# Optimization experiments

Hardware: AMD Instinct MI355X
Metric: run time of the kernel (lower is better)

Reference implementation:

```python
import jax, jax.numpy as jnp
import numpy as np

VOCAB, D_MODEL, N_STATE, H_HEADS, LAYERS = 64, 512, 32, 16, 4
EXPAND = 2
D_INNER = EXPAND * D_MODEL          # 1024
P_HEAD = D_INNER // H_HEADS         # 64
CONV_DIM = D_INNER + 2 * N_STATE    # x, B, C share the depthwise conv
K_CONV = 4
D_IN_PROJ = 2 * D_INNER + 2 * N_STATE + H_HEADS  # z, x, B, C, dt
BATCH, SEQ = 4, 1024
EPS = 1e-5


def rmsnorm(x, w):
    return x * jax.lax.rsqrt(jnp.mean(x * x, axis=-1, keepdims=True) + EPS) * w


def silu(x):
    return x * jax.nn.sigmoid(x)


def causal_depthwise_conv(x, w, b):
    # x: [B,L,C], w: [C,K], b: [C]; causal (left) padding, depthwise groups
    xt = jnp.transpose(x, (0, 2, 1))  # [B,C,L]
    out = jax.lax.conv_general_dilated(xt, w[:, None, :], (1,), [(K_CONV - 1, 0)], feature_group_count=w.shape[0])
    return jnp.transpose(out, (0, 2, 1)) + b


def ssd(xh, dt, A, Bm, Cm, Dp):
    # Mamba2 SSD recurrence. xh [B,L,H,P], dt [B,L,H], A [H], Bm/Cm [B,L,N], Dp [H]
    dA = jnp.exp(dt * A)              # decay per (batch, step, head)
    dtx = dt[..., None] * xh          # [B,L,H,P]

    def step(h, inp):
        dA_t, dtx_t, B_t, C_t = inp
        # h: [B,H,P,N]
        h = dA_t[:, :, None, None] * h + dtx_t[..., None] * B_t[:, None, None, :]
        y = jnp.einsum('bhpn,bn->bhp', h, C_t)
        return h, y

    h0 = jnp.zeros((xh.shape[0], H_HEADS, P_HEAD, N_STATE), xh.dtype)
    _, ys = jax.lax.scan(step, h0, (jnp.moveaxis(dA, 1, 0), jnp.moveaxis(dtx, 1, 0), jnp.moveaxis(Bm, 1, 0), jnp.moveaxis(Cm, 1, 0)))
    return jnp.moveaxis(ys, 0, 1) + xh * Dp[None, None, :, None]


def mamba_block(x, norm_w, W_in, b_in, conv_w, conv_b, dt_bias, A_log, Dp, gnorm_w, W_out, b_out):
    res = x
    u = rmsnorm(x, norm_w)
    zxbcdt = u @ W_in + b_in                                # [B,L,D_IN_PROJ]
    z = zxbcdt[..., :D_INNER]
    xBC = zxbcdt[..., D_INNER:D_INNER + CONV_DIM]
    dt = zxbcdt[..., D_INNER + CONV_DIM:]                   # [B,L,H]
    xBC = silu(causal_depthwise_conv(xBC, conv_w, conv_b))
    xc = xBC[..., :D_INNER]
    Bm = xBC[..., D_INNER:D_INNER + N_STATE]
    Cm = xBC[..., D_INNER + N_STATE:]
    dt = jax.nn.softplus(dt + dt_bias)
    xh = xc.reshape(xc.shape[0], xc.shape[1], H_HEADS, P_HEAD)
    y = ssd(xh, dt, -jnp.exp(A_log), Bm, Cm, Dp)
    y = y.reshape(y.shape[0], y.shape[1], D_INNER)
    y = rmsnorm(y * silu(z), gnorm_w)                       # gated RMSNorm
    return res + y @ W_out + b_out


def forward(input_tokens, emb, norm_w, W_in, b_in, conv_w, conv_b, dt_bias, A_log, D_param, gnorm_w, W_out, b_out, head_w, head_b):
    h = emb[input_tokens]
    for i in range(LAYERS):
        h = mamba_block(h, norm_w[i], W_in[i], b_in[i], conv_w[i], conv_b[i], dt_bias[i], A_log[i], D_param[i], gnorm_w[i], W_out[i], b_out[i])
    return h @ head_w + head_b


def setup_inputs() -> dict:
    key = jax.random.key(0)
    ks = jax.random.split(key, 8)
    s = 0.02
    return {
        'input_tokens': jax.random.randint(ks[0], (BATCH, SEQ), 0, VOCAB),
        'emb': jax.random.normal(ks[1], (VOCAB, D_MODEL), jnp.float32) * s,
        'norm_w': jnp.ones((LAYERS, D_MODEL), jnp.float32),
        'W_in': jax.random.normal(ks[2], (LAYERS, D_MODEL, D_IN_PROJ), jnp.float32) * s,
        'b_in': jnp.zeros((LAYERS, D_IN_PROJ), jnp.float32),
        'conv_w': jax.random.normal(ks[3], (LAYERS, CONV_DIM, K_CONV), jnp.float32) * 0.1,
        'conv_b': jnp.zeros((LAYERS, CONV_DIM), jnp.float32),
        'dt_bias': jnp.tile(jnp.log(jnp.expm1(jnp.linspace(0.001, 0.1, H_HEADS, dtype=jnp.float32))), (LAYERS, 1)),
        'A_log': jnp.tile(jnp.log(jnp.arange(1, H_HEADS + 1, dtype=jnp.float32)), (LAYERS, 1)),
        'D_param': jnp.ones((LAYERS, H_HEADS), jnp.float32),
        'gnorm_w': jnp.ones((LAYERS, D_INNER), jnp.float32),
        'W_out': jax.random.normal(ks[4], (LAYERS, D_INNER, D_MODEL), jnp.float32) * s,
        'b_out': jnp.zeros((LAYERS, D_MODEL), jnp.float32),
        'head_w': jax.random.normal(ks[5], (D_MODEL, VOCAB), jnp.float32) * s,
        'head_b': jnp.zeros((VOCAB,), jnp.float32),
    }


def reference(input_tokens, emb, norm_w, W_in, b_in, conv_w, conv_b, dt_bias, A_log, D_param, gnorm_w, W_out, b_out, head_w, head_b):
    return forward(input_tokens, emb, norm_w, W_in, b_in, conv_w, conv_b, dt_bias, A_log, D_param, gnorm_w, W_out, b_out, head_w, head_b)
```

## Files before the change

kernel.cpp:

```cpp
#include <hip/hip_runtime.h>
#include <hip/hip_bf16.h>

#define VOCAB     64
#define D_MODEL   512
#define N_STATE   32
#define H_HEADS   16
#define LAYERS    4
#define D_INNER   1024
#define P_HEAD    64
#define CONV_DIM  1088
#define K_CONV    4
#define D_IN_PROJ 2128
#define NPAD_IN   2176
#define NPAD_HEAD 128
#define BATCH     4
#define SEQ       1024
#define NTOK      (BATCH*SEQ)
#define EPS       1e-5f
#define CL        64
#define NC        (SEQ/CL)
#define PSTR      80

typedef __bf16 bf16x8 __attribute__((ext_vector_type(8)));
typedef float  f32x4  __attribute__((ext_vector_type(4)));

__device__ __forceinline__ float sigmoidf_(float x) { return 1.f / (1.f + __expf(-x)); }
__device__ __forceinline__ float softplusf_(float x) { return (x > 20.f) ? x : log1pf(__expf(x)); }

__global__ void rmsnorm512_kernel(const float* __restrict__ x, const float* __restrict__ w,
                                  __bf16* __restrict__ out,
                                  const int* __restrict__ tok, const float* __restrict__ emb,
                                  float* __restrict__ hout) {
  int tokid = blockIdx.x;
  int tid = threadIdx.x;
  float v0, v1;
  if (tok) {
    const float* er = emb + (size_t)tok[tokid] * D_MODEL;
    v0 = er[tid]; v1 = er[tid + 256];
    float* hr = hout + (size_t)tokid * D_MODEL;
    hr[tid] = v0; hr[tid + 256] = v1;
  } else {
    const float* xr = x + (size_t)tokid * D_MODEL;
    v0 = xr[tid]; v1 = xr[tid + 256];
  }
  float ss = v0 * v0 + v1 * v1;
  #pragma unroll
  for (int o = 32; o >= 1; o >>= 1) ss += __shfl_xor(ss, o);
  __shared__ float red[4];
  if ((tid & 63) == 0) red[tid >> 6] = ss;
  __syncthreads();
  float tot = red[0] + red[1] + red[2] + red[3];
  float sc = rsqrtf(tot * (1.f / D_MODEL) + EPS);
  out[(size_t)tokid * D_MODEL + tid]       = (__bf16)(v0 * sc * w[tid]);
  out[(size_t)tokid * D_MODEL + tid + 256] = (__bf16)(v1 * sc * w[tid + 256]);
}

__global__ void transpose_cast_kernel(const float* __restrict__ W, __bf16* __restrict__ Wt,
                                      int K, int N, int Npad) {
  W  += (size_t)blockIdx.z * K * N;
  Wt += (size_t)blockIdx.z * Npad * K;
  __shared__ float T[32][33];
  int n0 = blockIdx.x * 32, k0 = blockIdx.y * 32;
  int tx = threadIdx.x & 31, ty = threadIdx.x >> 5;
  #pragma unroll
  for (int i = 0; i < 4; i++) {
    int n = n0 + tx;
    T[ty + i * 8][tx] = (n < N) ? W[(size_t)(k0 + ty + i * 8) * N + n] : 0.f;
  }
  __syncthreads();
  #pragma unroll
  for (int i = 0; i < 4; i++)
    Wt[(size_t)(n0 + ty + i * 8) * K + k0 + tx] = (__bf16)T[tx][ty + i * 8];
}

#define TM 64
#define TN 128
#define TK 64
__global__ __launch_bounds__(256) void gemm_bf16_kernel(
    const __bf16* __restrict__ A, const __bf16* __restrict__ Bt,
    const float* __restrict__ bias, const float* __restrict__ res,
    float* __restrict__ C, __bf16* __restrict__ Cbf, int K, int N, int ldc) {
  __shared__ __bf16 As[TM * TK];
  __shared__ __bf16 Bs[TN * TK];
  int tid = threadIdx.x;
  int lane = tid & 63, wave = tid >> 6;
  int wm = wave >> 1, wn = wave & 1;
  int q = lane >> 4, l16 = lane & 15;
  size_t row0 = (size_t)blockIdx.y * TM;
  int col0 = blockIdx.x * TN;
  const __bf16* Ab = A + row0 * K;
  const __bf16* Bb = Bt + (size_t)col0 * K;

  bf16x8 pa[2], pb[4];
  #pragma unroll
  for (int r = 0; r < 2; r++) {
    int lin = r * 256 + tid;
    pa[r] = *(const bf16x8*)(Ab + (size_t)(lin >> 3) * K + (lin & 7) * 8);
  }
  #pragma unroll
  for (int r = 0; r < 4; r++) {
    int lin = r * 256 + tid;
    pb[r] = *(const bf16x8*)(Bb + (size_t)(lin >> 3) * K + (lin & 7) * 8);
  }

  f32x4 acc[2][4];
  #pragma unroll
  for (int i = 0; i < 2; i++)
    #pragma unroll
    for (int j = 0; j < 4; j++) acc[i][j] = (f32x4){0.f, 0.f, 0.f, 0.f};

  for (int k0 = 0; k0 < K; k0 += TK) {
    #pragma unroll
    for (int r = 0; r < 2; r++) { int lin = r * 256 + tid; *(bf16x8*)(As + lin * 8) = pa[r]; }
    #pragma unroll
    for (int r = 0; r < 4; r++) { int lin = r * 256 + tid; *(bf16x8*)(Bs + lin * 8) = pb[r]; }
    __syncthreads();
    int kn = k0 + TK;
    if (kn < K) {
      #pragma unroll
      for (int r = 0; r < 2; r++) {
        int lin = r * 256 + tid;
        pa[r] = *(const bf16x8*)(Ab + (size_t)(lin >> 3) * K + kn + (lin & 7) * 8);
      }
      #pragma unroll
      for (int r = 0; r < 4; r++) {
        int lin = r * 256 + tid;
        pb[r] = *(const bf16x8*)(Bb + (size_t)(lin >> 3) * K + kn + (lin & 7) * 8);
      }
    }
    #pragma unroll
    for (int ks = 0; ks < 2; ks++) {
      bf16x8 af[2], bfv[4];
      #pragma unroll
      for (int i = 0; i < 2; i++)
        af[i] = *(const bf16x8*)(As + (wm * 32 + i * 16 + l16) * TK + ks * 32 + q * 8);
      #pragma unroll
      for (int j = 0; j < 4; j++)
        bfv[j] = *(const bf16x8*)(Bs + (wn * 64 + j * 16 + l16) * TK + ks * 32 + q * 8);
      #pragma unroll
      for (int i = 0; i < 2; i++)
        #pragma unroll
        for (int j = 0; j < 4; j++)
          acc[i][j] = __builtin_amdgcn_mfma_f32_16x16x32_bf16(af[i], bfv[j], acc[i][j], 0, 0, 0);
    }
    __syncthreads();
  }

  #pragma unroll
  for (int i = 0; i < 2; i++) {
    size_t mrow = row0 + wm * 32 + i * 16 + q * 4;
    #pragma unroll
    for (int j = 0; j < 4; j++) {
      int col = col0 + wn * 64 + j * 16 + l16;
      if (col < N) {
        float bv = bias ? bias[col] : 0.f;
        #pragma unroll
        for (int rr = 0; rr < 4; rr++) {
          size_t off = (mrow + rr) * (size_t)ldc + col;
          float v = acc[i][j][rr] + bv;
          if (res) v += res[off];
          if (C)   C[off] = v;
          if (Cbf) Cbf[off] = (__bf16)v;
        }
      }
    }
  }
}

__global__ __launch_bounds__(256) void gemm_bf16_128(
    const __bf16* __restrict__ A, const __bf16* __restrict__ Bt,
    const float* __restrict__ bias, __bf16* __restrict__ Cbf,
    int K, int N, int ldc) {
  __shared__ __bf16 As[128 * TK];
  __shared__ __bf16 Bs[128 * TK];
  int tid = threadIdx.x;
  int lane = tid & 63, wave = tid >> 6;
  int wm = wave >> 1, wn = wave & 1;
  int q = lane >> 4, l16 = lane & 15;
  size_t row0 = (size_t)blockIdx.y * 128;
  int col0 = blockIdx.x * 128;
  const __bf16* Ab = A + row0 * K;
  const __bf16* Bb = Bt + (size_t)col0 * K;

  bf16x8 pa[4], pb[4];
  #pragma unroll
  for (int r = 0; r < 4; r++) {
    int lin = r * 256 + tid;
    pa[r] = *(const bf16x8*)(Ab + (size_t)(lin >> 3) * K + (lin & 7) * 8);
    pb[r] = *(const bf16x8*)(Bb + (size_t)(lin >> 3) * K + (lin & 7) * 8);
  }

  f32x4 acc[4][4];
  #pragma unroll
  for (int i = 0; i < 4; i++)
    #pragma unroll
    for (int j = 0; j < 4; j++) acc[i][j] = (f32x4){0.f, 0.f, 0.f, 0.f};

  for (int k0 = 0; k0 < K; k0 += TK) {
    #pragma unroll
    for (int r = 0; r < 4; r++) {
      int lin = r * 256 + tid;
      *(bf16x8*)(As + lin * 8) = pa[r];
      *(bf16x8*)(Bs + lin * 8) = pb[r];
    }
    __syncthreads();
    int kn = k0 + TK;
    if (kn < K) {
      #pragma unroll
      for (int r = 0; r < 4; r++) {
        int lin = r * 256 + tid;
        pa[r] = *(const bf16x8*)(Ab + (size_t)(lin >> 3) * K + kn + (lin & 7) * 8);
        pb[r] = *(const bf16x8*)(Bb + (size_t)(lin >> 3) * K + kn + (lin & 7) * 8);
      }
    }
    #pragma unroll
    for (int ks = 0; ks < 2; ks++) {
      bf16x8 af[4], bfv[4];
      #pragma unroll
      for (int i = 0; i < 4; i++)
        af[i] = *(const bf16x8*)(As + (wm * 64 + i * 16 + l16) * TK + ks * 32 + q * 8);
      #pragma unroll
      for (int j = 0; j < 4; j++)
        bfv[j] = *(const bf16x8*)(Bs + (wn * 64 + j * 16 + l16) * TK + ks * 32 + q * 8);
      #pragma unroll
      for (int i = 0; i < 4; i++)
        #pragma unroll
        for (int j = 0; j < 4; j++)
          acc[i][j] = __builtin_amdgcn_mfma_f32_16x16x32_bf16(af[i], bfv[j], acc[i][j], 0, 0, 0);
    }
    __syncthreads();
  }

  #pragma unroll
  for (int i = 0; i < 4; i++) {
    size_t mrow = row0 + wm * 64 + i * 16 + q * 4;
    #pragma unroll
    for (int j = 0; j < 4; j++) {
      int col = col0 + wn * 64 + j * 16 + l16;
      if (col < N) {
        float bv = bias[col];
        #pragma unroll
        for (int rr = 0; rr < 4; rr++)
          Cbf[(mrow + rr) * (size_t)ldc + col] = (__bf16)(acc[i][j][rr] + bv);
      }
    }
  }
}

__device__ __forceinline__ void wave0_dt_cumsum(
    const __bf16* __restrict__ zxbf, const float* __restrict__ dt_bias,
    int b, int h, int t0, int tid, float* ldt, float* lcs) {
  if (tid < 64) {
    float dv = (float)zxbf[((size_t)(b * SEQ + t0 + tid)) * D_IN_PROJ + 2 * D_INNER + 2 * N_STATE + h]
               + dt_bias[h];
    float dtv = softplusf_(dv);
    float cs = dtv;
    #pragma unroll
    for (int off = 1; off < 64; off <<= 1) {
      float o = __shfl_up(cs, off);
      if (tid >= off) cs += o;
    }
    ldt[tid] = dtv;
    lcs[tid] = cs;
  }
}

__global__ __launch_bounds__(256) void ssd_local_kernel(
    const __bf16* __restrict__ zxbf, const float* __restrict__ conv_w,
    const float* __restrict__ conv_b, const float* __restrict__ dt_bias,
    const float* __restrict__ A_log,
    float* __restrict__ Slocal, float* __restrict__ dAprod) {
  int blk = blockIdx.x;
  int c = blk % NC;
  int h = (blk / NC) % H_HEADS;
  int b = blk / (NC * H_HEADS);
  int tid = threadIdx.x;
  int lane = tid & 63, wave = tid >> 6;
  int q = lane >> 4, l16 = lane & 15;
  int t0 = c * CL;
  float A = -__expf(A_log[h]);
  __shared__ __bf16 rawx[68][64];
  __shared__ __bf16 rawB[68][32];
  __shared__ __bf16 lxT[64][PSTR];
  __shared__ __bf16 lBT[32][PSTR];
  __shared__ float ldt[64], lcs[64];
  for (int i = tid; i < 68 * 8; i += 256) {
    int r = i >> 3, c0 = (i & 7) * 8;
    int gr = t0 - 3 + r;
    bf16x8 v;
    #pragma unroll
    for (int k = 0; k < 8; k++) v[k] = (__bf16)0.f;
    if (gr >= 0)
      v = *(const bf16x8*)(zxbf + ((size_t)(b * SEQ + gr)) * D_IN_PROJ + D_INNER + h * 64 + c0);
    *(bf16x8*)(&rawx[r][c0]) = v;
  }
  for (int i = tid; i < 68 * 4; i += 256) {
    int r = i >> 2, c0 = (i & 3) * 8;
    int gr = t0 - 3 + r;
    bf16x8 v;
    #pragma unroll
    for (int k = 0; k < 8; k++) v[k] = (__bf16)0.f;
    if (gr >= 0)
      v = *(const bf16x8*)(zxbf + ((size_t)(b * SEQ + gr)) * D_IN_PROJ + 2 * D_INNER + c0);
    *(bf16x8*)(&rawB[r][c0]) = v;
  }
  wave0_dt_cumsum(zxbf, dt_bias, b, h, t0, tid, ldt, lcs);
  __syncthreads();
  float cs63 = lcs[63];
  {
    int p = tid & 63;
    const float* w = conv_w + (h * 64 + p) * K_CONV;
    float w0 = w[0], w1 = w[1], w2 = w[2], w3 = w[3];
    float cb = conv_b[h * 64 + p];
    for (int i = tid; i < CL * 64; i += 256) {
      int t = i >> 6;
      float a = cb + w0 * (float)rawx[t][p] + w1 * (float)rawx[t + 1][p]
                   + w2 * (float)rawx[t + 2][p] + w3 * (float)rawx[t + 3][p];
      lxT[p][t] = (__bf16)(a * sigmoidf_(a));
    }
  }
  {
    int n = tid & 31;
    const float* w = conv_w + (D_INNER + n) * K_CONV;
    float w0 = w[0], w1 = w[1], w2 = w[2], w3 = w[3];
    float cb = conv_b[D_INNER + n];
    for (int i = tid; i < CL * 32; i += 256) {
      int t = i >> 5;
      float a = cb + w0 * (float)rawB[t][n] + w1 * (float)rawB[t + 1][n]
                   + w2 * (float)rawB[t + 2][n] + w3 * (float)rawB[t + 3][n];
      float v = a * sigmoidf_(a);
      float wt = ldt[t] * __expf(A * (cs63 - lcs[t]));
      lBT[n][t] = (__bf16)(v * wt);
    }
  }
  __syncthreads();
  f32x4 acc[2];
  acc[0] = (f32x4){0.f,0.f,0.f,0.f}; acc[1] = (f32x4){0.f,0.f,0.f,0.f};
  #pragma unroll
  for (int kb = 0; kb < 2; kb++) {
    bf16x8 af = *(const bf16x8*)(&lxT[wave * 16 + l16][kb * 32 + q * 8]);
    #pragma unroll
    for (int j = 0; j < 2; j++) {
      bf16x8 bf = *(const bf16x8*)(&lBT[l16 + 16 * j][kb * 32 + q * 8]);
      acc[j] = __builtin_amdgcn_mfma_f32_16x16x32_bf16(af, bf, acc[j], 0, 0, 0);
    }
  }
  float* dst = Slocal + (size_t)blk * 2048;
  #pragma unroll
  for (int j = 0; j < 2; j++) {
    int n = l16 + 16 * j;
    #pragma unroll
    for (int rr = 0; rr < 4; rr++) {
      int p = wave * 16 + q * 4 + rr;
      dst[p * 32 + n] = acc[j][rr];
    }
  }
  if (tid == 0) dAprod[blk] = __expf(A * cs63);
}

__global__ __launch_bounds__(256) void ssd_out_kernel(
    const __bf16* __restrict__ zxbf, const float* __restrict__ conv_w,
    const float* __restrict__ conv_b, const float* __restrict__ dt_bias,
    const float* __restrict__ A_log, const float* __restrict__ Dp,
    const float* __restrict__ Slocal, const float* __restrict__ dAprod,
    __bf16* __restrict__ y) {
  int blk = blockIdx.x;
  int c = blk % NC;
  int h = (blk / NC) % H_HEADS;
  int b = blk / (NC * H_HEADS);
  int tid = threadIdx.x;
  int lane = tid & 63, wave = tid >> 6;
  int q = lane >> 4, l16 = lane & 15;
  int t0 = c * CL;
  float A = -__expf(A_log[h]);
  float D = Dp[h];
  __shared__ __bf16 rawbuf[2 * 68 * 64];
  __shared__ __bf16 lxT[64][PSTR];
  __shared__ __bf16 lB[64][32];
  __shared__ __bf16 lC[64][32];
  __shared__ __bf16 lS[64][32];
  __shared__ float ldt[64], lcs[64];
  __shared__ float pr[NC];
  __bf16* rawx = rawbuf;
  __bf16* rawBC = rawbuf + 68 * 64;
  for (int i = tid; i < 68 * 8; i += 256) {
    int r = i >> 3, c0 = (i & 7) * 8;
    int gr = t0 - 3 + r;
    bf16x8 vx, vbc;
    #pragma unroll
    for (int k = 0; k < 8; k++) { vx[k] = (__bf16)0.f; vbc[k] = (__bf16)0.f; }
    if (gr >= 0) {
      const __bf16* rowp = zxbf + ((size_t)(b * SEQ + gr)) * D_IN_PROJ;
      vx  = *(const bf16x8*)(rowp + D_INNER + h * 64 + c0);
      vbc = *(const bf16x8*)(rowp + 2 * D_INNER + c0);
    }
    *(bf16x8*)(rawx + r * 64 + c0)  = vx;
    *(bf16x8*)(rawBC + r * 64 + c0) = vbc;
  }
  if (tid < NC) pr[tid] = dAprod[(blk - c) + tid];
  wave0_dt_cumsum(zxbf, dt_bias, b, h, t0, tid, ldt, lcs);
  __syncthreads();
  {
    int p = tid & 63;
    const float* w = conv_w + (h * 64 + p) * K_CONV;
    float w0 = w[0], w1 = w[1], w2 = w[2], w3 = w[3];
    float cb = conv_b[h * 64 + p];
    for (int i = tid; i < CL * 64; i += 256) {
      int t = i >> 6;
      float a = cb + w0 * (float)rawx[t * 64 + p] + w1 * (float)rawx[(t + 1) * 64 + p]
                   + w2 * (float)rawx[(t + 2) * 64 + p] + w3 * (float)rawx[(t + 3) * 64 + p];
      lxT[p][t] = (__bf16)(a * sigmoidf_(a));
    }
  }
  {
    int col = tid & 63;
    const float* w = conv_w + (D_INNER + col) * K_CONV;
    float w0 = w[0], w1 = w[1], w2 = w[2], w3 = w[3];
    float cb = conv_b[D_INNER + col];
    for (int i = tid; i < CL * 64; i += 256) {
      int t = i >> 6;
      float a = cb + w0 * (float)rawBC[t * 64 + col] + w1 * (float)rawBC[(t + 1) * 64 + col]
                   + w2 * (float)rawBC[(t + 2) * 64 + col] + w3 * (float)rawBC[(t + 3) * 64 + col];
      float v = a * sigmoidf_(a);
      if (col < 32) lB[t][col] = (__bf16)v; else lC[t][col - 32] = (__bf16)v;
    }
  }
  {
    int p = tid >> 2, n0 = (tid & 3) * 8;
    const float* sl = Slocal + (size_t)(blk - c) * 2048 + p * 32 + n0;
    float st[8] = {};
    for (int j = 0; j < c; j++) {
      f32x4 a = *(const f32x4*)(sl + (size_t)j * 2048);
      f32x4 bq = *(const f32x4*)(sl + (size_t)j * 2048 + 4);
      float prj = pr[j];
      #pragma unroll
      for (int k = 0; k < 4; k++) { st[k] = prj * st[k] + a[k]; st[4 + k] = prj * st[4 + k] + bq[k]; }
    }
    #pragma unroll
    for (int k = 0; k < 8; k++) lS[p][n0 + k] = (__bf16)st[k];
  }
  __syncthreads();
  bf16x8 afC = *(const bf16x8*)(&lC[wave * 16 + l16][q * 8]);
  f32x4 accG[4], accI[4], accY[4];
  #pragma unroll
  for (int j = 0; j < 4; j++) {
    accG[j] = (f32x4){0.f,0.f,0.f,0.f};
    accI[j] = (f32x4){0.f,0.f,0.f,0.f};
    accY[j] = (f32x4){0.f,0.f,0.f,0.f};
  }
  #pragma unroll
  for (int j = 0; j < 4; j++) {
    bf16x8 bf = *(const bf16x8*)(&lB[l16 + 16 * j][q * 8]);
    accG[j] = __builtin_amdgcn_mfma_f32_16x16x32_bf16(afC, bf, accG[j], 0, 0, 0);
  }
  #pragma unroll
  for (int j = 0; j < 4; j++) {
    bf16x8 bf = *(const bf16x8*)(&lS[l16 + 16 * j][q * 8]);
    accI[j] = __builtin_amdgcn_mfma_f32_16x16x32_bf16(afC, bf, accI[j], 0, 0, 0);
  }
  __bf16* pP = rawbuf + wave * 16 * PSTR;
  #pragma unroll
  for (int j = 0; j < 4; j++) {
    int s = l16 + 16 * j;
    float css = lcs[s], dts = ldt[s];
    #pragma unroll
    for (int rr = 0; rr < 4; rr++) {
      int tl = q * 4 + rr;
      int t = wave * 16 + tl;
      float val = accG[j][rr] * __expf(A * (lcs[t] - css)) * dts;
      if (s == t) val += D;
      if (s > t) val = 0.f;
      pP[tl * PSTR + s] = (__bf16)val;
    }
  }
  #pragma unroll
  for (int kb = 0; kb < 2; kb++) {
    bf16x8 afP = *(const bf16x8*)(pP + l16 * PSTR + kb * 32 + q * 8);
    #pragma unroll
    for (int j = 0; j < 4; j++) {
      bf16x8 bf = *(const bf16x8*)(&lxT[l16 + 16 * j][kb * 32 + q * 8]);
      accY[j] = __builtin_amdgcn_mfma_f32_16x16x32_bf16(afP, bf, accY[j], 0, 0, 0);
    }
  }
  #pragma unroll
  for (int rr = 0; rr < 4; rr++) {
    int t = wave * 16 + q * 4 + rr;
    float cumt = __expf(A * lcs[t]);
    __bf16* yrow = y + ((size_t)(b * SEQ + t0 + t)) * D_INNER + h * 64;
    #pragma unroll
    for (int j = 0; j < 4; j++) {
      int p = l16 + 16 * j;
      yrow[p] = (__bf16)(accY[j][rr] + cumt * accI[j][rr]);
    }
  }
}

__global__ void gate_norm_kernel(const __bf16* __restrict__ zxbf, const float* __restrict__ gw,
                                 const __bf16* __restrict__ y, __bf16* __restrict__ ybf) {
  int tok = blockIdx.x;
  int tid = threadIdx.x;
  const __bf16* zr = zxbf + (size_t)tok * D_IN_PROJ;
  const __bf16* yr = y + (size_t)tok * D_INNER;
  float v[4];
  float ss = 0.f;
  #pragma unroll
  for (int i = 0; i < 4; i++) {
    int d = tid + i * 256;
    float z = (float)zr[d];
    float g = (float)yr[d] * z * sigmoidf_(z);
    v[i] = g;
    ss += g * g;
  }
  #pragma unroll
  for (int o = 32; o >= 1; o >>= 1) ss += __shfl_xor(ss, o);
  __shared__ float red[4];
  if ((tid & 63) == 0) red[tid >> 6] = ss;
  __syncthreads();
  float tot = red[0] + red[1] + red[2] + red[3];
  float sc = rsqrtf(tot * (1.f / D_INNER) + EPS);
  #pragma unroll
  for (int i = 0; i < 4; i++) {
    int d = tid + i * 256;
    ybf[(size_t)tok * D_INNER + d] = (__bf16)(v[i] * sc * gw[d]);
  }
}

extern "C" void kernel_launch(void* const* d_in, const int* in_sizes, int n_in,
                              void* d_out, int out_size, void* d_ws, size_t ws_size,
                              hipStream_t stream) {
  const int*   tok     = (const int*)  d_in[0];
  const float* emb     = (const float*)d_in[1];
  const float* norm_w  = (const float*)d_in[2];
  const float* W_in    = (const float*)d_in[3];
  const float* b_in    = (const float*)d_in[4];
  const float* conv_w  = (const float*)d_in[5];
  const float* conv_b  = (const float*)d_in[6];
  const float* dt_bias = (const float*)d_in[7];
  const float* A_log   = (const float*)d_in[8];
  const float* D_par   = (const float*)d_in[9];
  const float* gnorm_w = (const float*)d_in[10];
  const float* W_out   = (const float*)d_in[11];
  const float* b_out   = (const float*)d_in[12];
  const float* head_w  = (const float*)d_in[13];
  const float* head_b  = (const float*)d_in[14];
  float* out = (float*)d_out;

  char* p = (char*)d_ws;
  auto alloc = [&](size_t bytes) { void* r = (void*)p; p += (bytes + 255) & ~(size_t)255; return r; };
  float*  h      = (float*) alloc((size_t)NTOK * D_MODEL * 4);
  float*  slocal = (float*) alloc((size_t)BATCH * H_HEADS * NC * P_HEAD * N_STATE * 4);
  float*  daprod = (float*) alloc((size_t)BATCH * H_HEADS * NC * 4);
  __bf16* y      = (__bf16*)alloc((size_t)NTOK * D_INNER * 2);
  __bf16* zxbf   = (__bf16*)alloc((size_t)NTOK * D_IN_PROJ * 2);
  __bf16* ubf    = (__bf16*)alloc((size_t)NTOK * D_MODEL * 2);
  __bf16* ybf    = (__bf16*)alloc((size_t)NTOK * D_INNER * 2);
  __bf16* hbf    = (__bf16*)alloc((size_t)NTOK * D_MODEL * 2);
  __bf16* WtIn   = (__bf16*)alloc((size_t)LAYERS * NPAD_IN * D_MODEL * 2);
  __bf16* WtOut  = (__bf16*)alloc((size_t)LAYERS * D_MODEL * D_INNER * 2);
  __bf16* WtHead = (__bf16*)alloc((size_t)NPAD_HEAD * D_MODEL * 2);

  transpose_cast_kernel<<<dim3(NPAD_IN / 32, D_MODEL / 32, LAYERS), 256, 0, stream>>>(
      W_in, WtIn, D_MODEL, D_IN_PROJ, NPAD_IN);
  transpose_cast_kernel<<<dim3(D_MODEL / 32, D_INNER / 32, LAYERS), 256, 0, stream>>>(
      W_out, WtOut, D_INNER, D_MODEL, D_MODEL);
  transpose_cast_kernel<<<dim3(NPAD_HEAD / 32, D_MODEL / 32, 1), 256, 0, stream>>>(
      head_w, WtHead, D_MODEL, VOCAB, NPAD_HEAD);

  for (int l = 0; l < LAYERS; l++) {
    rmsnorm512_kernel<<<NTOK, 256, 0, stream>>>(
        h, norm_w + (size_t)l * D_MODEL, ubf,
        (l == 0) ? tok : nullptr, (l == 0) ? emb : nullptr, h);

    gemm_bf16_128<<<dim3(NPAD_IN / 128, NTOK / 128), 256, 0, stream>>>(
        ubf, WtIn + (size_t)l * NPAD_IN * D_MODEL, b_in + (size_t)l * D_IN_PROJ,
        zxbf, D_MODEL, D_IN_PROJ, D_IN_PROJ);

    ssd_local_kernel<<<BATCH * H_HEADS * NC, 256, 0, stream>>>(
        zxbf, conv_w + (size_t)l * CONV_DIM * K_CONV, conv_b + (size_t)l * CONV_DIM,
        dt_bias + (size_t)l * H_HEADS, A_log + (size_t)l * H_HEADS, slocal, daprod);
    ssd_out_kernel<<<BATCH * H_HEADS * NC, 256, 0, stream>>>(
        zxbf, conv_w + (size_t)l * CONV_DIM * K_CONV, conv_b + (size_t)l * CONV_DIM,
        dt_bias + (size_t)l * H_HEADS, A_log + (size_t)l * H_HEADS,
        D_par + (size_t)l * H_HEADS, slocal, daprod, y);

    gate_norm_kernel<<<NTOK, 256, 0, stream>>>(zxbf, gnorm_w + (size_t)l * D_INNER, y, ybf);

    gemm_bf16_kernel<<<dim3(D_MODEL / TN, NTOK / TM), 256, 0, stream>>>(
        ybf, WtOut + (size_t)l * D_MODEL * D_INNER, b_out + (size_t)l * D_MODEL, h, h,
        (l == LAYERS - 1) ? hbf : nullptr, D_INNER, D_MODEL, D_MODEL);
  }

  gemm_bf16_kernel<<<dim3(NPAD_HEAD / TN, NTOK / TM), 256, 0, stream>>>(
      hbf, WtHead, head_b, nullptr, out, nullptr, D_MODEL, VOCAB, VOCAB);
}
```

Measured before the change: 494.6 us.

## Load GEMM tiles directly to LDS and shrink output-projection tile to 64x64

```diff
diff --git a/kernel.cpp b/kernel.cpp
--- a/kernel.cpp
+++ b/kernel.cpp
@@ -12,7 +12,7 @@
 #define K_CONV    4
 #define D_IN_PROJ 2128
 #define NPAD_IN   2176
-#define NPAD_HEAD 128
+#define NPAD_HEAD 64
 #define BATCH     4
 #define SEQ       1024
 #define NTOK      (BATCH*SEQ)
@@ -26,6 +26,12 @@
 
 __device__ __forceinline__ float sigmoidf_(float x) { return 1.f / (1.f + __expf(-x)); }
 __device__ __forceinline__ float softplusf_(float x) { return (x > 20.f) ? x : log1pf(__expf(x)); }
+
+__device__ __forceinline__ void gload_lds16(const void* g, void* l) {
+  __builtin_amdgcn_global_load_lds((const __attribute__((address_space(1))) void*)g,
+                                   (__attribute__((address_space(3))) void*)l,
+                                   16, 0, 0);
+}
 
 __global__ void rmsnorm512_kernel(const float* __restrict__ x, const float* __restrict__ w,
                                   __bf16* __restrict__ out,
@@ -73,74 +79,50 @@
     Wt[(size_t)(n0 + ty + i * 8) * K + k0 + tx] = (__bf16)T[tx][ty + i * 8];
 }
 
-#define TM 64
-#define TN 128
 #define TK 64
 __global__ __launch_bounds__(256) void gemm_bf16_kernel(
     const __bf16* __restrict__ A, const __bf16* __restrict__ Bt,
     const float* __restrict__ bias, const float* __restrict__ res,
     float* __restrict__ C, __bf16* __restrict__ Cbf, int K, int N, int ldc) {
-  __shared__ __bf16 As[TM * TK];
-  __shared__ __bf16 Bs[TN * TK];
+  __shared__ __bf16 As[64 * TK];
+  __shared__ __bf16 Bs[64 * TK];
   int tid = threadIdx.x;
   int lane = tid & 63, wave = tid >> 6;
   int wm = wave >> 1, wn = wave & 1;
   int q = lane >> 4, l16 = lane & 15;
-  size_t row0 = (size_t)blockIdx.y * TM;
-  int col0 = blockIdx.x * TN;
+  size_t row0 = (size_t)blockIdx.y * 64;
+  int col0 = blockIdx.x * 64;
   const __bf16* Ab = A + row0 * K;
   const __bf16* Bb = Bt + (size_t)col0 * K;
 
-  bf16x8 pa[2], pb[4];
-  #pragma unroll
-  for (int r = 0; r < 2; r++) {
-    int lin = r * 256 + tid;
-    pa[r] = *(const bf16x8*)(Ab + (size_t)(lin >> 3) * K + (lin & 7) * 8);
-  }
-  #pragma unroll
-  for (int r = 0; r < 4; r++) {
-    int lin = r * 256 + tid;
-    pb[r] = *(const bf16x8*)(Bb + (size_t)(lin >> 3) * K + (lin & 7) * 8);
-  }
-
-  f32x4 acc[2][4];
+  f32x4 acc[2][2];
   #pragma unroll
   for (int i = 0; i < 2; i++)
     #pragma unroll
-    for (int j = 0; j < 4; j++) acc[i][j] = (f32x4){0.f, 0.f, 0.f, 0.f};
+    for (int j = 0; j < 2; j++) acc[i][j] = (f32x4){0.f, 0.f, 0.f, 0.f};
 
   for (int k0 = 0; k0 < K; k0 += TK) {
     #pragma unroll
-    for (int r = 0; r < 2; r++) { int lin = r * 256 + tid; *(bf16x8*)(As + lin * 8) = pa[r]; }
-    #pragma unroll
-    for (int r = 0; r < 4; r++) { int lin = r * 256 + tid; *(bf16x8*)(Bs + lin * 8) = pb[r]; }
+    for (int r = 0; r < 2; r++) {
+      int lin = r * 256 + tid;
+      size_t goff = (size_t)(lin >> 3) * K + k0 + (lin & 7) * 8;
+      gload_lds16(Ab + goff, As + lin * 8);
+      gload_lds16(Bb + goff, Bs + lin * 8);
+    }
     __syncthreads();
-    int kn = k0 + TK;
-    if (kn < K) {
-      #pragma unroll
-      for (int r = 0; r < 2; r++) {
-        int lin = r * 256 + tid;
-        pa[r] = *(const bf16x8*)(Ab + (size_t)(lin >> 3) * K + kn + (lin & 7) * 8);
-      }
-      #pragma unroll
-      for (int r = 0; r < 4; r++) {
-        int lin = r * 256 + tid;
-        pb[r] = *(const bf16x8*)(Bb + (size_t)(lin >> 3) * K + kn + (lin & 7) * 8);
-      }
-    }
     #pragma unroll
     for (int ks = 0; ks < 2; ks++) {
-      bf16x8 af[2], bfv[4];
+      bf16x8 af[2], bfv[2];
       #pragma unroll
       for (int i = 0; i < 2; i++)
         af[i] = *(const bf16x8*)(As + (wm * 32 + i * 16 + l16) * TK + ks * 32 + q * 8);
       #pragma unroll
-      for (int j = 0; j < 4; j++)
-        bfv[j] = *(const bf16x8*)(Bs + (wn * 64 + j * 16 + l16) * TK + ks * 32 + q * 8);
+      for (int j = 0; j < 2; j++)
+        bfv[j] = *(const bf16x8*)(Bs + (wn * 32 + j * 16 + l16) * TK + ks * 32 + q * 8);
       #pragma unroll
       for (int i = 0; i < 2; i++)
         #pragma unroll
-        for (int j = 0; j < 4; j++)
+        for (int j = 0; j < 2; j++)
           acc[i][j] = __builtin_amdgcn_mfma_f32_16x16x32_bf16(af[i], bfv[j], acc[i][j], 0, 0, 0);
     }
     __syncthreads();
@@ -150,8 +132,8 @@
   for (int i = 0; i < 2; i++) {
     size_t mrow = row0 + wm * 32 + i * 16 + q * 4;
     #pragma unroll
-    for (int j = 0; j < 4; j++) {
-      int col = col0 + wn * 64 + j * 16 + l16;
+    for (int j = 0; j < 2; j++) {
+      int col = col0 + wn * 32 + j * 16 + l16;
       if (col < N) {
         float bv = bias ? bias[col] : 0.f;
         #pragma unroll
@@ -182,14 +164,6 @@
   const __bf16* Ab = A + row0 * K;
   const __bf16* Bb = Bt + (size_t)col0 * K;
 
-  bf16x8 pa[4], pb[4];
-  #pragma unroll
-  for (int r = 0; r < 4; r++) {
-    int lin = r * 256 + tid;
-    pa[r] = *(const bf16x8*)(Ab + (size_t)(lin >> 3) * K + (lin & 7) * 8);
-    pb[r] = *(const bf16x8*)(Bb + (size_t)(lin >> 3) * K + (lin & 7) * 8);
-  }
-
   f32x4 acc[4][4];
   #pragma unroll
   for (int i = 0; i < 4; i++)
@@ -200,19 +174,11 @@
     #pragma unroll
     for (int r = 0; r < 4; r++) {
       int lin = r * 256 + tid;
-      *(bf16x8*)(As + lin * 8) = pa[r];
-      *(bf16x8*)(Bs + lin * 8) = pb[r];
+      size_t goff = (size_t)(lin >> 3) * K + k0 + (lin & 7) * 8;
+      gload_lds16(Ab + goff, As + lin * 8);
+      gload_lds16(Bb + goff, Bs + lin * 8);
     }
     __syncthreads();
-    int kn = k0 + TK;
-    if (kn < K) {
-      #pragma unroll
-      for (int r = 0; r < 4; r++) {
-        int lin = r * 256 + tid;
-        pa[r] = *(const bf16x8*)(Ab + (size_t)(lin >> 3) * K + kn + (lin & 7) * 8);
-        pb[r] = *(const bf16x8*)(Bb + (size_t)(lin >> 3) * K + kn + (lin & 7) * 8);
-      }
-    }
     #pragma unroll
     for (int ks = 0; ks < 2; ks++) {
       bf16x8 af[4], bfv[4];
@@ -585,11 +551,11 @@
 
     gate_norm_kernel<<<NTOK, 256, 0, stream>>>(zxbf, gnorm_w + (size_t)l * D_INNER, y, ybf);
 
-    gemm_bf16_kernel<<<dim3(D_MODEL / TN, NTOK / TM), 256, 0, stream>>>(
+    gemm_bf16_kernel<<<dim3(D_MODEL / 64, NTOK / 64), 256, 0, stream>>>(
         ybf, WtOut + (size_t)l * D_MODEL * D_INNER, b_out + (size_t)l * D_MODEL, h, h,
         (l == LAYERS - 1) ? hbf : nullptr, D_INNER, D_MODEL, D_MODEL);
   }
 
-  gemm_bf16_kernel<<<dim3(NPAD_HEAD / TN, NTOK / TM), 256, 0, stream>>>(
+  gemm_bf16_kernel<<<dim3(NPAD_HEAD / 64, NTOK / 64), 256, 0, stream>>>(
       hbf, WtHead, head_b, nullptr, out, nullptr, D_MODEL, VOCAB, VOCAB);
 }
```

After: 490.0 us. No clear change (-0.9%).
